# Performance work log

Measured on AMD Instinct MI355X. Metric: run time of the kernel, lower is better.

## Reference

```python
import jax, jax.numpy as jnp
import numpy as np

H = 64  # hidden size

def _lstm_layer(x_btf, w_ih, w_hh, b_ih, b_hh):
    """One LSTM layer, batch_first input x_btf [B,T,F]. PyTorch gate order i,f,g,o."""
    B = x_btf.shape[0]
    # Precompute input contribution for all timesteps: [T,B,4H]
    xg = jnp.einsum('btf,gf->tbg', x_btf, w_ih) + (b_ih + b_hh)
    h0 = jnp.zeros((B, H), dtype=x_btf.dtype)
    c0 = jnp.zeros((B, H), dtype=x_btf.dtype)

    def step(carry, xg_t):
        h, c = carry
        gates = xg_t + h @ w_hh.T  # [B,4H]
        i, f, g, o = jnp.split(gates, 4, axis=-1)
        i = jax.nn.sigmoid(i)
        f = jax.nn.sigmoid(f)
        g = jnp.tanh(g)
        o = jax.nn.sigmoid(o)
        c_new = f * c + i * g
        h_new = o * jnp.tanh(c_new)
        return (h_new, c_new), h_new

    (h_T, c_T), hs = jax.lax.scan(step, (h0, c0), xg)
    return jnp.transpose(hs, (1, 0, 2)), h_T, c_T  # [B,T,H], [B,H], [B,H]


def setup_inputs() -> dict:
    key = jax.random.key(0)
    ks = jax.random.split(key, 9)
    s_in = 1.0 / np.sqrt(H)
    inp = {
        'x': jax.random.normal(ks[0], (512, 2048, 4), dtype=jnp.float32),
        'w_ih_l0': jax.random.uniform(ks[1], (4 * H, 4), jnp.float32, -s_in, s_in),
        'w_hh_l0': jax.random.uniform(ks[2], (4 * H, H), jnp.float32, -s_in, s_in),
        'b_ih_l0': jax.random.uniform(ks[3], (4 * H,), jnp.float32, -s_in, s_in),
        'b_hh_l0': jax.random.uniform(ks[4], (4 * H,), jnp.float32, -s_in, s_in),
        'w_ih_l1': jax.random.uniform(ks[5], (4 * H, H), jnp.float32, -s_in, s_in),
        'w_hh_l1': jax.random.uniform(ks[6], (4 * H, H), jnp.float32, -s_in, s_in),
        'b_ih_l1': jax.random.uniform(ks[7], (4 * H,), jnp.float32, -s_in, s_in),
        'b_hh_l1': jax.random.uniform(ks[8], (4 * H,), jnp.float32, -s_in, s_in),
    }
    return inp


def reference(x, w_ih_l0, w_hh_l0, b_ih_l0, b_hh_l0, w_ih_l1, w_hh_l1, b_ih_l1, b_hh_l1):
    out0, h0, c0 = _lstm_layer(x, w_ih_l0, w_hh_l0, b_ih_l0, b_hh_l0)
    out1, h1, c1 = _lstm_layer(out0, w_ih_l1, w_hh_l1, b_ih_l1, b_hh_l1)
    h_n = jnp.stack([h0, h1], axis=0)  # [num_layers, B, H]
    c_n = jnp.stack([c0, c1], axis=0)
    return out1, (h_n, c_n)
```

## Files before the change

### kernel.cpp

```cpp
#include <hip/hip_runtime.h>

#define T_STEPS 2048
#define HID 64

typedef __attribute__((ext_vector_type(8))) short short8;
typedef __attribute__((ext_vector_type(4))) float f32x4;

static __device__ __forceinline__ unsigned short f2bf(float f) {
    unsigned int uu = __float_as_uint(f);
    uu = uu + 0x7fffu + ((uu >> 16) & 1u);
    return (unsigned short)(uu >> 16);
}
static __device__ __forceinline__ float exp2_f(float x) {
#if __has_builtin(__builtin_amdgcn_exp2f)
    return __builtin_amdgcn_exp2f(x);
#else
    return exp2f(x);
#endif
}
static __device__ __forceinline__ float sig2(float s) {
    return __builtin_amdgcn_rcpf(1.0f + exp2_f(s));
}
static __device__ __forceinline__ float tanh2(float s) {
    return fmaf(2.0f, __builtin_amdgcn_rcpf(1.0f + exp2_f(s)), -1.0f);
}
#define NLOG2E 1.4426950408889634f

__global__ void __launch_bounds__(512, 1) __attribute__((amdgpu_waves_per_eu(2, 2)))
lstm2_ws2(const float* __restrict__ x,
          const float* __restrict__ wih0, const float* __restrict__ whh0,
          const float* __restrict__ bih0, const float* __restrict__ bhh0,
          const float* __restrict__ wih1, const float* __restrict__ whh1,
          const float* __restrict__ bih1, const float* __restrict__ bhh1,
          float* __restrict__ out, int B)
{
    __shared__ __align__(16) unsigned short s_h0[2][2][HID];
    __shared__ __align__(16) unsigned short s_h1[2][2][HID];
    __shared__ __align__(16) float s_xf[2 * T_STEPS * 4];

    const int tid  = threadIdx.x;
    const int lane = tid & 63;
    const int wv   = tid >> 6;
    const int wg   = wv >> 2;
    const int wl   = wv & 3;
    const int l15  = lane & 15;
    const int lg   = lane >> 4;
    const int b0   = 2 * blockIdx.x;
    const int u    = 16 * wl + l15;
    const int bx   = lg & 1;
    const int rsel = (l15 >> 2) & 1;

    const float SCL[4] = {-NLOG2E, -NLOG2E, -2.0f * NLOG2E, -NLOG2E};

    const float4* __restrict__ xb4 = (const float4*)(x + (size_t)b0 * (T_STEPS * 4));
    float4* s_xf4 = (float4*)s_xf;
    for (int i2 = tid; i2 < 2 * T_STEPS; i2 += 512) s_xf4[i2] = xb4[i2];
    if (tid < 256) {
        ((unsigned short*)s_h0)[tid] = 0;
        ((unsigned short*)s_h1)[tid] = 0;
    }

    const size_t BTH = (size_t)B * T_STEPS * HID;
    const size_t BH  = (size_t)B * HID;
    const size_t bi  = (size_t)(b0 + bx) * HID + u;
    const f32x4 Z = {0.f, 0.f, 0.f, 0.f};

    #define BAR() do { asm volatile("s_waitcnt lgkmcnt(0)" ::: "memory"); \
                       __builtin_amdgcn_s_barrier(); } while (0)

    if (wg == 0) {
        short8 W0[4][2];
        float  wx[4][4];
        f32x4  Bias0[4];
        #pragma unroll
        for (int ni = 0; ni < 4; ++ni) {
            const int g = 64 * ni + u;
            const float sc = SCL[ni];
            #pragma unroll
            for (int kt = 0; kt < 2; ++kt)
                #pragma unroll
                for (int j = 0; j < 8; ++j)
                    W0[ni][kt][j] = (short)f2bf(whh0[g * HID + kt * 32 + lg * 8 + j] * sc);
            #pragma unroll
            for (int j = 0; j < 4; ++j) wx[ni][j] = wih0[g * 4 + j] * sc;
            const float bb = (bih0[g] + bhh0[g]) * sc;
            Bias0[ni] = (f32x4){bb, bb, bb, bb};
        }
        float c0s = 0.f, h0s = 0.f;
        const float* xcur = &s_xf[(size_t)bx * T_STEPS * 4];
        __syncthreads();

        auto l0_body = [&](int P) {
            const int Q = P ^ 1;
            const short8 Ha = *(const short8*)&s_h0[Q][rsel][8 * lg];
            const short8 Hb = *(const short8*)&s_h0[Q][rsel][32 + 8 * lg];
            const float4 xt = *(const float4*)xcur;  xcur += 4;
            __builtin_amdgcn_s_setprio(1);
            f32x4 aA0 = __builtin_amdgcn_mfma_f32_16x16x32_bf16(Ha, W0[0][0], Bias0[0], 0, 0, 0);
            f32x4 aA1 = __builtin_amdgcn_mfma_f32_16x16x32_bf16(Ha, W0[1][0], Bias0[1], 0, 0, 0);
            f32x4 aA2 = __builtin_amdgcn_mfma_f32_16x16x32_bf16(Ha, W0[2][0], Bias0[2], 0, 0, 0);
            f32x4 aA3 = __builtin_amdgcn_mfma_f32_16x16x32_bf16(Ha, W0[3][0], Bias0[3], 0, 0, 0);
            f32x4 aB0 = __builtin_amdgcn_mfma_f32_16x16x32_bf16(Hb, W0[0][1], Z, 0, 0, 0);
            f32x4 aB1 = __builtin_amdgcn_mfma_f32_16x16x32_bf16(Hb, W0[1][1], Z, 0, 0, 0);
            f32x4 aB2 = __builtin_amdgcn_mfma_f32_16x16x32_bf16(Hb, W0[2][1], Z, 0, 0, 0);
            f32x4 aB3 = __builtin_amdgcn_mfma_f32_16x16x32_bf16(Hb, W0[3][1], Z, 0, 0, 0);
            __builtin_amdgcn_s_setprio(0);
            float s0 = aA0[0] + aB0[0];
            float s1 = aA1[0] + aB1[0];
            float s2 = aA2[0] + aB2[0];
            float s3 = aA3[0] + aB3[0];
            s0 = fmaf(wx[0][0], xt.x, s0); s0 = fmaf(wx[0][1], xt.y, s0);
            s0 = fmaf(wx[0][2], xt.z, s0); s0 = fmaf(wx[0][3], xt.w, s0);
            s1 = fmaf(wx[1][0], xt.x, s1); s1 = fmaf(wx[1][1], xt.y, s1);
            s1 = fmaf(wx[1][2], xt.z, s1); s1 = fmaf(wx[1][3], xt.w, s1);
            s2 = fmaf(wx[2][0], xt.x, s2); s2 = fmaf(wx[2][1], xt.y, s2);
            s2 = fmaf(wx[2][2], xt.z, s2); s2 = fmaf(wx[2][3], xt.w, s2);
            s3 = fmaf(wx[3][0], xt.x, s3); s3 = fmaf(wx[3][1], xt.y, s3);
            s3 = fmaf(wx[3][2], xt.z, s3); s3 = fmaf(wx[3][3], xt.w, s3);
            float i_ = sig2(s0);
            float f_ = sig2(s1);
            float g_ = tanh2(s2);
            float o_ = sig2(s3);
            c0s = fmaf(f_, c0s, i_ * g_);
            h0s = o_ * tanh2(c0s * (-2.0f * NLOG2E));
            if (lg < 2) s_h0[P][lg][u] = f2bf(h0s);
        };

        for (int it = 0; it < T_STEPS / 2; ++it) {
            l0_body(0); BAR();
            l0_body(1); BAR();
        }
        if (lg < 2) {
            out[BTH + bi]          = h0s;
            out[BTH + 2 * BH + bi] = c0s;
        }
    } else {
        short8 W1[4][4];
        f32x4  Bias1[4];
        #pragma unroll
        for (int ni = 0; ni < 4; ++ni) {
            const int g = 64 * ni + u;
            const float sc = SCL[ni];
            #pragma unroll
            for (int kt = 0; kt < 2; ++kt)
                #pragma unroll
                for (int j = 0; j < 8; ++j) {
                    W1[ni][kt][j]     = (short)f2bf(wih1[g * HID + kt * 32 + lg * 8 + j] * sc);
                    W1[ni][2 + kt][j] = (short)f2bf(whh1[g * HID + kt * 32 + lg * 8 + j] * sc);
                }
            const float bb = (bih1[g] + bhh1[g]) * sc;
            Bias1[ni] = (f32x4){bb, bb, bb, bb};
        }
        float c1s = 0.f, h1s = 0.f;
        float* __restrict__ opp = out + (size_t)(b0 + bx) * T_STEPS * HID + u;
        __syncthreads();
        BAR();

        auto l1_body = [&](int P) {
            const int Q = P ^ 1;
            const short8 Ha = *(const short8*)&s_h0[Q][rsel][8 * lg];
            const short8 Hb = *(const short8*)&s_h0[Q][rsel][32 + 8 * lg];
            const short8 Ga = *(const short8*)&s_h1[Q][rsel][8 * lg];
            const short8 Gb = *(const short8*)&s_h1[Q][rsel][32 + 8 * lg];
            __builtin_amdgcn_s_setprio(1);
            f32x4 dH0 = __builtin_amdgcn_mfma_f32_16x16x32_bf16(Ha, W1[0][0], Bias1[0], 0, 0, 0);
            f32x4 dH1 = __builtin_amdgcn_mfma_f32_16x16x32_bf16(Ha, W1[1][0], Bias1[1], 0, 0, 0);
            f32x4 dH2 = __builtin_amdgcn_mfma_f32_16x16x32_bf16(Ha, W1[2][0], Bias1[2], 0, 0, 0);
            f32x4 dH3 = __builtin_amdgcn_mfma_f32_16x16x32_bf16(Ha, W1[3][0], Bias1[3], 0, 0, 0);
            f32x4 dG0 = __builtin_amdgcn_mfma_f32_16x16x32_bf16(Ga, W1[0][2], Z, 0, 0, 0);
            f32x4 dG1 = __builtin_amdgcn_mfma_f32_16x16x32_bf16(Ga, W1[1][2], Z, 0, 0, 0);
            f32x4 dG2 = __builtin_amdgcn_mfma_f32_16x16x32_bf16(Ga, W1[2][2], Z, 0, 0, 0);
            f32x4 dG3 = __builtin_amdgcn_mfma_f32_16x16x32_bf16(Ga, W1[3][2], Z, 0, 0, 0);
            dH0 = __builtin_amdgcn_mfma_f32_16x16x32_bf16(Hb, W1[0][1], dH0, 0, 0, 0);
            dH1 = __builtin_amdgcn_mfma_f32_16x16x32_bf16(Hb, W1[1][1], dH1, 0, 0, 0);
            dH2 = __builtin_amdgcn_mfma_f32_16x16x32_bf16(Hb, W1[2][1], dH2, 0, 0, 0);
            dH3 = __builtin_amdgcn_mfma_f32_16x16x32_bf16(Hb, W1[3][1], dH3, 0, 0, 0);
            dG0 = __builtin_amdgcn_mfma_f32_16x16x32_bf16(Gb, W1[0][3], dG0, 0, 0, 0);
            dG1 = __builtin_amdgcn_mfma_f32_16x16x32_bf16(Gb, W1[1][3], dG1, 0, 0, 0);
            dG2 = __builtin_amdgcn_mfma_f32_16x16x32_bf16(Gb, W1[2][3], dG2, 0, 0, 0);
            dG3 = __builtin_amdgcn_mfma_f32_16x16x32_bf16(Gb, W1[3][3], dG3, 0, 0, 0);
            __builtin_amdgcn_s_setprio(0);
            float i_ = sig2(dH0[0] + dG0[0]);
            float f_ = sig2(dH1[0] + dG1[0]);
            float g_ = tanh2(dH2[0] + dG2[0]);
            float o_ = sig2(dH3[0] + dG3[0]);
            c1s = fmaf(f_, c1s, i_ * g_);
            h1s = o_ * tanh2(c1s * (-2.0f * NLOG2E));
            if (lg < 2) {
                s_h1[P][lg][u] = f2bf(h1s);
                *opp = h1s;
            }
            opp += HID;
        };

        for (int it = 0; it < T_STEPS / 2 - 1; ++it) {
            l1_body(1); BAR();
            l1_body(0); BAR();
        }
        l1_body(1); BAR();
        l1_body(0);
        if (lg < 2) {
            out[BTH + BH + bi]     = h1s;
            out[BTH + 3 * BH + bi] = c1s;
        }
    }
    #undef BAR
}

extern "C" void kernel_launch(void* const* d_in, const int* in_sizes, int n_in,
                              void* d_out, int out_size, void* d_ws, size_t ws_size,
                              hipStream_t stream) {
    const float* x    = (const float*)d_in[0];
    const float* wih0 = (const float*)d_in[1];
    const float* whh0 = (const float*)d_in[2];
    const float* bih0 = (const float*)d_in[3];
    const float* bhh0 = (const float*)d_in[4];
    const float* wih1 = (const float*)d_in[5];
    const float* whh1 = (const float*)d_in[6];
    const float* bih1 = (const float*)d_in[7];
    const float* bhh1 = (const float*)d_in[8];
    float* out = (float*)d_out;

    const int B = in_sizes[0] / (T_STEPS * 4);

    lstm2_ws2<<<dim3(B / 2), dim3(512), 0, stream>>>(
        x, wih0, whh0, bih0, bhh0, wih1, whh1, bih1, bhh1, out, B);
}
```

Measured before the change: 719.8 us.

## Replace lockstep barriers with LDS counter dataflow sync between LSTM layers

```diff
diff --git a/kernel.cpp b/kernel.cpp
--- a/kernel.cpp
+++ b/kernel.cpp
@@ -27,15 +27,16 @@
 #define NLOG2E 1.4426950408889634f
 
 __global__ void __launch_bounds__(512, 1) __attribute__((amdgpu_waves_per_eu(2, 2)))
-lstm2_ws2(const float* __restrict__ x,
-          const float* __restrict__ wih0, const float* __restrict__ whh0,
-          const float* __restrict__ bih0, const float* __restrict__ bhh0,
-          const float* __restrict__ wih1, const float* __restrict__ whh1,
-          const float* __restrict__ bih1, const float* __restrict__ bhh1,
-          float* __restrict__ out, int B)
+lstm2_df(const float* __restrict__ x,
+         const float* __restrict__ wih0, const float* __restrict__ whh0,
+         const float* __restrict__ bih0, const float* __restrict__ bhh0,
+         const float* __restrict__ wih1, const float* __restrict__ whh1,
+         const float* __restrict__ bih1, const float* __restrict__ bhh1,
+         float* __restrict__ out, int B)
 {
-    __shared__ __align__(16) unsigned short s_h0[2][2][HID];
-    __shared__ __align__(16) unsigned short s_h1[2][2][HID];
+    __shared__ __align__(16) unsigned short s_h0[4][2][HID];
+    __shared__ __align__(16) unsigned short s_h1[4][2][HID];
+    __shared__ __align__(8)  unsigned s_cnt[2];
     __shared__ __align__(16) float s_xf[2 * T_STEPS * 4];
 
     const int tid  = threadIdx.x;
@@ -56,17 +57,34 @@
     float4* s_xf4 = (float4*)s_xf;
     for (int i2 = tid; i2 < 2 * T_STEPS; i2 += 512) s_xf4[i2] = xb4[i2];
     if (tid < 256) {
-        ((unsigned short*)s_h0)[tid] = 0;
-        ((unsigned short*)s_h1)[tid] = 0;
+        ((unsigned short*)s_h0)[tid] = 0; ((unsigned short*)s_h0)[tid + 256] = 0;
+        ((unsigned short*)s_h1)[tid] = 0; ((unsigned short*)s_h1)[tid + 256] = 0;
     }
+    if (tid == 0) { s_cnt[0] = 0; s_cnt[1] = 0; }
+    __syncthreads();
 
     const size_t BTH = (size_t)B * T_STEPS * HID;
     const size_t BH  = (size_t)B * HID;
     const size_t bi  = (size_t)(b0 + bx) * HID + u;
     const f32x4 Z = {0.f, 0.f, 0.f, 0.f};
 
-    #define BAR() do { asm volatile("s_waitcnt lgkmcnt(0)" ::: "memory"); \
-                       __builtin_amdgcn_s_barrier(); } while (0)
+    auto poll2 = [&](int T0, int T1) {
+        if (T0 <= 0 && T1 <= 0) return;
+        const unsigned uT0 = (T0 > 0) ? (unsigned)T0 : 0u;
+        const unsigned uT1 = (T1 > 0) ? (unsigned)T1 : 0u;
+        volatile unsigned long long* pc = (volatile unsigned long long*)&s_cnt[0];
+        unsigned long long cc = *pc;
+        while ((unsigned)cc < uT0 || (unsigned)(cc >> 32) < uT1) {
+            __builtin_amdgcn_s_sleep(1);
+            cc = *pc;
+        }
+        asm volatile("s_waitcnt lgkmcnt(0)" ::: "memory");
+        __builtin_amdgcn_sched_barrier(0);
+    };
+    auto publish = [&](int which) {
+        asm volatile("s_waitcnt lgkmcnt(0)" ::: "memory");
+        if (lane == 0) atomicAdd(&s_cnt[which], 1u);
+    };
 
     if (wg == 0) {
         short8 W0[4][2];
@@ -88,10 +106,10 @@
         }
         float c0s = 0.f, h0s = 0.f;
         const float* xcur = &s_xf[(size_t)bx * T_STEPS * 4];
-        __syncthreads();
-
-        auto l0_body = [&](int P) {
-            const int Q = P ^ 1;
+
+        auto l0_step = [&](int t, int P) {
+            const int Q = (P + 3) & 3;
+            poll2(4 * t, 4 * (t - 3));
             const short8 Ha = *(const short8*)&s_h0[Q][rsel][8 * lg];
             const short8 Hb = *(const short8*)&s_h0[Q][rsel][32 + 8 * lg];
             const float4 xt = *(const float4*)xcur;  xcur += 4;
@@ -124,11 +142,15 @@
             c0s = fmaf(f_, c0s, i_ * g_);
             h0s = o_ * tanh2(c0s * (-2.0f * NLOG2E));
             if (lg < 2) s_h0[P][lg][u] = f2bf(h0s);
+            publish(0);
         };
 
-        for (int it = 0; it < T_STEPS / 2; ++it) {
-            l0_body(0); BAR();
-            l0_body(1); BAR();
+        for (int it = 0; it < T_STEPS / 4; ++it) {
+            const int tb = 4 * it;
+            l0_step(tb + 0, 0);
+            l0_step(tb + 1, 1);
+            l0_step(tb + 2, 2);
+            l0_step(tb + 3, 3);
         }
         if (lg < 2) {
             out[BTH + bi]          = h0s;
@@ -153,13 +175,12 @@
         }
         float c1s = 0.f, h1s = 0.f;
         float* __restrict__ opp = out + (size_t)(b0 + bx) * T_STEPS * HID + u;
-        __syncthreads();
-        BAR();
-
-        auto l1_body = [&](int P) {
-            const int Q = P ^ 1;
-            const short8 Ha = *(const short8*)&s_h0[Q][rsel][8 * lg];
-            const short8 Hb = *(const short8*)&s_h0[Q][rsel][32 + 8 * lg];
+
+        auto l1_step = [&](int s, int P) {
+            const int Q = (P + 3) & 3;
+            poll2(4 * (s + 1), 4 * s);
+            const short8 Ha = *(const short8*)&s_h0[P][rsel][8 * lg];
+            const short8 Hb = *(const short8*)&s_h0[P][rsel][32 + 8 * lg];
             const short8 Ga = *(const short8*)&s_h1[Q][rsel][8 * lg];
             const short8 Gb = *(const short8*)&s_h1[Q][rsel][32 + 8 * lg];
             __builtin_amdgcn_s_setprio(1);
@@ -191,20 +212,21 @@
                 *opp = h1s;
             }
             opp += HID;
+            publish(1);
         };
 
-        for (int it = 0; it < T_STEPS / 2 - 1; ++it) {
-            l1_body(1); BAR();
-            l1_body(0); BAR();
-        }
-        l1_body(1); BAR();
-        l1_body(0);
+        for (int it = 0; it < T_STEPS / 4; ++it) {
+            const int sb = 4 * it;
+            l1_step(sb + 0, 0);
+            l1_step(sb + 1, 1);
+            l1_step(sb + 2, 2);
+            l1_step(sb + 3, 3);
+        }
         if (lg < 2) {
             out[BTH + BH + bi]     = h1s;
             out[BTH + 3 * BH + bi] = c1s;
         }
     }
-    #undef BAR
 }
 
 extern "C" void kernel_launch(void* const* d_in, const int* in_sizes, int n_in,
@@ -223,6 +245,6 @@
 
     const int B = in_sizes[0] / (T_STEPS * 4);
 
-    lstm2_ws2<<<dim3(B / 2), dim3(512), 0, stream>>>(
+    lstm2_df<<<dim3(B / 2), dim3(512), 0, stream>>>(
         x, wih0, whh0, bih0, bhh0, wih1, whh1, bih1, bhh1, out, B);
 }
```

Result: slower. 993.4 us (+38.0%).

## Quantize LSTM recurrent matmuls to int8 MFMA with per-row weight scales

Applied to the files above, without the earlier changes.

```diff
diff --git a/kernel.cpp b/kernel.cpp
--- a/kernel.cpp
+++ b/kernel.cpp
@@ -3,14 +3,9 @@
 #define T_STEPS 2048
 #define HID 64
 
-typedef __attribute__((ext_vector_type(8))) short short8;
+typedef __attribute__((ext_vector_type(4))) int   int4v;
 typedef __attribute__((ext_vector_type(4))) float f32x4;
 
-static __device__ __forceinline__ unsigned short f2bf(float f) {
-    unsigned int uu = __float_as_uint(f);
-    uu = uu + 0x7fffu + ((uu >> 16) & 1u);
-    return (unsigned short)(uu >> 16);
-}
 static __device__ __forceinline__ float exp2_f(float x) {
 #if __has_builtin(__builtin_amdgcn_exp2f)
     return __builtin_amdgcn_exp2f(x);
@@ -18,24 +13,18 @@
     return exp2f(x);
 #endif
 }
-static __device__ __forceinline__ float sig2(float s) {
-    return __builtin_amdgcn_rcpf(1.0f + exp2_f(s));
-}
-static __device__ __forceinline__ float tanh2(float s) {
-    return fmaf(2.0f, __builtin_amdgcn_rcpf(1.0f + exp2_f(s)), -1.0f);
-}
 #define NLOG2E 1.4426950408889634f
 
 __global__ void __launch_bounds__(512, 1) __attribute__((amdgpu_waves_per_eu(2, 2)))
-lstm2_ws2(const float* __restrict__ x,
-          const float* __restrict__ wih0, const float* __restrict__ whh0,
-          const float* __restrict__ bih0, const float* __restrict__ bhh0,
-          const float* __restrict__ wih1, const float* __restrict__ whh1,
-          const float* __restrict__ bih1, const float* __restrict__ bhh1,
-          float* __restrict__ out, int B)
+lstm2_i8(const float* __restrict__ x,
+         const float* __restrict__ wih0, const float* __restrict__ whh0,
+         const float* __restrict__ bih0, const float* __restrict__ bhh0,
+         const float* __restrict__ wih1, const float* __restrict__ whh1,
+         const float* __restrict__ bih1, const float* __restrict__ bhh1,
+         float* __restrict__ out, int B)
 {
-    __shared__ __align__(16) unsigned short s_h0[2][2][HID];
-    __shared__ __align__(16) unsigned short s_h1[2][2][HID];
+    __shared__ __align__(16) char s_h0q[2][2][HID];
+    __shared__ __align__(16) char s_h1q[2][2][HID];
     __shared__ __align__(16) float s_xf[2 * T_STEPS * 4];
 
     const int tid  = threadIdx.x;
@@ -56,35 +45,58 @@
     float4* s_xf4 = (float4*)s_xf;
     for (int i2 = tid; i2 < 2 * T_STEPS; i2 += 512) s_xf4[i2] = xb4[i2];
     if (tid < 256) {
-        ((unsigned short*)s_h0)[tid] = 0;
-        ((unsigned short*)s_h1)[tid] = 0;
+        ((char*)s_h0q)[tid] = 0;
+        ((char*)s_h1q)[tid] = 0;
     }
 
     const size_t BTH = (size_t)B * T_STEPS * HID;
     const size_t BH  = (size_t)B * HID;
     const size_t bi  = (size_t)(b0 + bx) * HID + u;
-    const f32x4 Z = {0.f, 0.f, 0.f, 0.f};
+    const int4v Zi = {0, 0, 0, 0};
+
+    auto pack16 = [&](const float* wr, float qs) {
+        int4v r;
+        #pragma unroll
+        for (int dw = 0; dw < 4; ++dw) {
+            unsigned d = 0;
+            #pragma unroll
+            for (int bbb = 0; bbb < 4; ++bbb) {
+                int q = (int)rintf(wr[dw * 4 + bbb] * qs);
+                d |= ((unsigned)(q & 255)) << (8 * bbb);
+            }
+            r[dw] = (int)d;
+        }
+        return r;
+    };
+    auto rowmax = [&](const float* wr) {
+        float mx = 0.f;
+        #pragma unroll
+        for (int j = 0; j < 16; ++j) mx = fmaxf(mx, fabsf(wr[j]));
+        mx = fmaxf(mx, __shfl_xor(mx, 16));
+        mx = fmaxf(mx, __shfl_xor(mx, 32));
+        return fmaxf(mx, 1e-20f);
+    };
 
     #define BAR() do { asm volatile("s_waitcnt lgkmcnt(0)" ::: "memory"); \
                        __builtin_amdgcn_s_barrier(); } while (0)
 
     if (wg == 0) {
-        short8 W0[4][2];
-        float  wx[4][4];
-        f32x4  Bias0[4];
+        int4v W0q[4];
+        float dq0[4];
+        float wx[4][4];
+        float b0s[4];
         #pragma unroll
         for (int ni = 0; ni < 4; ++ni) {
             const int g = 64 * ni + u;
-            const float sc = SCL[ni];
-            #pragma unroll
-            for (int kt = 0; kt < 2; ++kt)
-                #pragma unroll
-                for (int j = 0; j < 8; ++j)
-                    W0[ni][kt][j] = (short)f2bf(whh0[g * HID + kt * 32 + lg * 8 + j] * sc);
-            #pragma unroll
-            for (int j = 0; j < 4; ++j) wx[ni][j] = wih0[g * 4 + j] * sc;
-            const float bb = (bih0[g] + bhh0[g]) * sc;
-            Bias0[ni] = (f32x4){bb, bb, bb, bb};
+            float wr[16];
+            #pragma unroll
+            for (int j = 0; j < 16; ++j) wr[j] = whh0[g * HID + 16 * lg + j];
+            float mx = rowmax(wr);
+            W0q[ni] = pack16(wr, 127.f / mx);
+            dq0[ni] = (mx / (127.f * 127.f)) * SCL[ni];
+            #pragma unroll
+            for (int j = 0; j < 4; ++j) wx[ni][j] = wih0[g * 4 + j] * SCL[ni];
+            b0s[ni] = (bih0[g] + bhh0[g]) * SCL[ni];
         }
         float c0s = 0.f, h0s = 0.f;
         const float* xcur = &s_xf[(size_t)bx * T_STEPS * 4];
@@ -92,38 +104,33 @@
 
         auto l0_body = [&](int P) {
             const int Q = P ^ 1;
-            const short8 Ha = *(const short8*)&s_h0[Q][rsel][8 * lg];
-            const short8 Hb = *(const short8*)&s_h0[Q][rsel][32 + 8 * lg];
+            const int4v Ha = *(const int4v*)&s_h0q[Q][rsel][16 * lg];
             const float4 xt = *(const float4*)xcur;  xcur += 4;
             __builtin_amdgcn_s_setprio(1);
-            f32x4 aA0 = __builtin_amdgcn_mfma_f32_16x16x32_bf16(Ha, W0[0][0], Bias0[0], 0, 0, 0);
-            f32x4 aA1 = __builtin_amdgcn_mfma_f32_16x16x32_bf16(Ha, W0[1][0], Bias0[1], 0, 0, 0);
-            f32x4 aA2 = __builtin_amdgcn_mfma_f32_16x16x32_bf16(Ha, W0[2][0], Bias0[2], 0, 0, 0);
-            f32x4 aA3 = __builtin_amdgcn_mfma_f32_16x16x32_bf16(Ha, W0[3][0], Bias0[3], 0, 0, 0);
-            f32x4 aB0 = __builtin_amdgcn_mfma_f32_16x16x32_bf16(Hb, W0[0][1], Z, 0, 0, 0);
-            f32x4 aB1 = __builtin_amdgcn_mfma_f32_16x16x32_bf16(Hb, W0[1][1], Z, 0, 0, 0);
-            f32x4 aB2 = __builtin_amdgcn_mfma_f32_16x16x32_bf16(Hb, W0[2][1], Z, 0, 0, 0);
-            f32x4 aB3 = __builtin_amdgcn_mfma_f32_16x16x32_bf16(Hb, W0[3][1], Z, 0, 0, 0);
+            int4v a0 = __builtin_amdgcn_mfma_i32_16x16x64_i8(Ha, W0q[0], Zi, 0, 0, 0);
+            int4v a1 = __builtin_amdgcn_mfma_i32_16x16x64_i8(Ha, W0q[1], Zi, 0, 0, 0);
+            int4v a2 = __builtin_amdgcn_mfma_i32_16x16x64_i8(Ha, W0q[2], Zi, 0, 0, 0);
+            int4v a3 = __builtin_amdgcn_mfma_i32_16x16x64_i8(Ha, W0q[3], Zi, 0, 0, 0);
             __builtin_amdgcn_s_setprio(0);
-            float s0 = aA0[0] + aB0[0];
-            float s1 = aA1[0] + aB1[0];
-            float s2 = aA2[0] + aB2[0];
-            float s3 = aA3[0] + aB3[0];
-            s0 = fmaf(wx[0][0], xt.x, s0); s0 = fmaf(wx[0][1], xt.y, s0);
-            s0 = fmaf(wx[0][2], xt.z, s0); s0 = fmaf(wx[0][3], xt.w, s0);
-            s1 = fmaf(wx[1][0], xt.x, s1); s1 = fmaf(wx[1][1], xt.y, s1);
-            s1 = fmaf(wx[1][2], xt.z, s1); s1 = fmaf(wx[1][3], xt.w, s1);
-            s2 = fmaf(wx[2][0], xt.x, s2); s2 = fmaf(wx[2][1], xt.y, s2);
-            s2 = fmaf(wx[2][2], xt.z, s2); s2 = fmaf(wx[2][3], xt.w, s2);
-            s3 = fmaf(wx[3][0], xt.x, s3); s3 = fmaf(wx[3][1], xt.y, s3);
-            s3 = fmaf(wx[3][2], xt.z, s3); s3 = fmaf(wx[3][3], xt.w, s3);
-            float i_ = sig2(s0);
-            float f_ = sig2(s1);
-            float g_ = tanh2(s2);
-            float o_ = sig2(s3);
+            float t0 = fmaf(wx[0][0], xt.x, b0s[0]);
+            float t1 = fmaf(wx[1][0], xt.x, b0s[1]);
+            float t2 = fmaf(wx[2][0], xt.x, b0s[2]);
+            float t3 = fmaf(wx[3][0], xt.x, b0s[3]);
+            t0 = fmaf(wx[0][1], xt.y, t0); t0 = fmaf(wx[0][2], xt.z, t0); t0 = fmaf(wx[0][3], xt.w, t0);
+            t1 = fmaf(wx[1][1], xt.y, t1); t1 = fmaf(wx[1][2], xt.z, t1); t1 = fmaf(wx[1][3], xt.w, t1);
+            t2 = fmaf(wx[2][1], xt.y, t2); t2 = fmaf(wx[2][2], xt.z, t2); t2 = fmaf(wx[2][3], xt.w, t2);
+            t3 = fmaf(wx[3][1], xt.y, t3); t3 = fmaf(wx[3][2], xt.z, t3); t3 = fmaf(wx[3][3], xt.w, t3);
+            float s0 = fmaf((float)a0[0], dq0[0], t0);
+            float s1 = fmaf((float)a1[0], dq0[1], t1);
+            float s2 = fmaf((float)a2[0], dq0[2], t2);
+            float s3 = fmaf((float)a3[0], dq0[3], t3);
+            float i_ = __builtin_amdgcn_rcpf(1.0f + exp2_f(s0));
+            float f_ = __builtin_amdgcn_rcpf(1.0f + exp2_f(s1));
+            float g_ = fmaf(2.0f, __builtin_amdgcn_rcpf(1.0f + exp2_f(s2)), -1.0f);
+            float o_ = __builtin_amdgcn_rcpf(1.0f + exp2_f(s3));
             c0s = fmaf(f_, c0s, i_ * g_);
-            h0s = o_ * tanh2(c0s * (-2.0f * NLOG2E));
-            if (lg < 2) s_h0[P][lg][u] = f2bf(h0s);
+            h0s = o_ * fmaf(2.0f, __builtin_amdgcn_rcpf(1.0f + exp2_f(c0s * (-2.0f * NLOG2E))), -1.0f);
+            if (lg < 2) s_h0q[P][lg][u] = (char)(int)rintf(h0s * 127.f);
         };
 
         for (int it = 0; it < T_STEPS / 2; ++it) {
@@ -135,21 +142,23 @@
             out[BTH + 2 * BH + bi] = c0s;
         }
     } else {
-        short8 W1[4][4];
-        f32x4  Bias1[4];
+        int4v Wihq[4], Whhq[4];
+        float dqih[4], dqhh[4], b1s[4];
         #pragma unroll
         for (int ni = 0; ni < 4; ++ni) {
             const int g = 64 * ni + u;
-            const float sc = SCL[ni];
-            #pragma unroll
-            for (int kt = 0; kt < 2; ++kt)
-                #pragma unroll
-                for (int j = 0; j < 8; ++j) {
-                    W1[ni][kt][j]     = (short)f2bf(wih1[g * HID + kt * 32 + lg * 8 + j] * sc);
-                    W1[ni][2 + kt][j] = (short)f2bf(whh1[g * HID + kt * 32 + lg * 8 + j] * sc);
-                }
-            const float bb = (bih1[g] + bhh1[g]) * sc;
-            Bias1[ni] = (f32x4){bb, bb, bb, bb};
+            float wr[16];
+            #pragma unroll
+            for (int j = 0; j < 16; ++j) wr[j] = wih1[g * HID + 16 * lg + j];
+            float mxi = rowmax(wr);
+            Wihq[ni] = pack16(wr, 127.f / mxi);
+            dqih[ni] = (mxi / (127.f * 127.f)) * SCL[ni];
+            #pragma unroll
+            for (int j = 0; j < 16; ++j) wr[j] = whh1[g * HID + 16 * lg + j];
+            float mxh = rowmax(wr);
+            Whhq[ni] = pack16(wr, 127.f / mxh);
+            dqhh[ni] = (mxh / (127.f * 127.f)) * SCL[ni];
+            b1s[ni] = (bih1[g] + bhh1[g]) * SCL[ni];
         }
         float c1s = 0.f, h1s = 0.f;
         float* __restrict__ opp = out + (size_t)(b0 + bx) * T_STEPS * HID + u;
@@ -158,36 +167,30 @@
 
         auto l1_body = [&](int P) {
             const int Q = P ^ 1;
-            const short8 Ha = *(const short8*)&s_h0[Q][rsel][8 * lg];
-            const short8 Hb = *(const short8*)&s_h0[Q][rsel][32 + 8 * lg];
-            const short8 Ga = *(const short8*)&s_h1[Q][rsel][8 * lg];
-            const short8 Gb = *(const short8*)&s_h1[Q][rsel][32 + 8 * lg];
+            const int4v Ha = *(const int4v*)&s_h0q[Q][rsel][16 * lg];
+            const int4v Ga = *(const int4v*)&s_h1q[Q][rsel][16 * lg];
             __builtin_amdgcn_s_setprio(1);
-            f32x4 dH0 = __builtin_amdgcn_mfma_f32_16x16x32_bf16(Ha, W1[0][0], Bias1[0], 0, 0, 0);
-            f32x4 dH1 = __builtin_amdgcn_mfma_f32_16x16x32_bf16(Ha, W1[1][0], Bias1[1], 0, 0, 0);
-            f32x4 dH2 = __builtin_amdgcn_mfma_f32_16x16x32_bf16(Ha, W1[2][0], Bias1[2], 0, 0, 0);
-            f32x4 dH3 = __builtin_amdgcn_mfma_f32_16x16x32_bf16(Ha, W1[3][0], Bias1[3], 0, 0, 0);
-            f32x4 dG0 = __builtin_amdgcn_mfma_f32_16x16x32_bf16(Ga, W1[0][2], Z, 0, 0, 0);
-            f32x4 dG1 = __builtin_amdgcn_mfma_f32_16x16x32_bf16(Ga, W1[1][2], Z, 0, 0, 0);
-            f32x4 dG2 = __builtin_amdgcn_mfma_f32_16x16x32_bf16(Ga, W1[2][2], Z, 0, 0, 0);
-            f32x4 dG3 = __builtin_amdgcn_mfma_f32_16x16x32_bf16(Ga, W1[3][2], Z, 0, 0, 0);
-            dH0 = __builtin_amdgcn_mfma_f32_16x16x32_bf16(Hb, W1[0][1], dH0, 0, 0, 0);
-            dH1 = __builtin_amdgcn_mfma_f32_16x16x32_bf16(Hb, W1[1][1], dH1, 0, 0, 0);
-            dH2 = __builtin_amdgcn_mfma_f32_16x16x32_bf16(Hb, W1[2][1], dH2, 0, 0, 0);
-            dH3 = __builtin_amdgcn_mfma_f32_16x16x32_bf16(Hb, W1[3][1], dH3, 0, 0, 0);
-            dG0 = __builtin_amdgcn_mfma_f32_16x16x32_bf16(Gb, W1[0][3], dG0, 0, 0, 0);
-            dG1 = __builtin_amdgcn_mfma_f32_16x16x32_bf16(Gb, W1[1][3], dG1, 0, 0, 0);
-            dG2 = __builtin_amdgcn_mfma_f32_16x16x32_bf16(Gb, W1[2][3], dG2, 0, 0, 0);
-            dG3 = __builtin_amdgcn_mfma_f32_16x16x32_bf16(Gb, W1[3][3], dG3, 0, 0, 0);
+            int4v dH0 = __builtin_amdgcn_mfma_i32_16x16x64_i8(Ha, Wihq[0], Zi, 0, 0, 0);
+            int4v dH1 = __builtin_amdgcn_mfma_i32_16x16x64_i8(Ha, Wihq[1], Zi, 0, 0, 0);
+            int4v dH2 = __builtin_amdgcn_mfma_i32_16x16x64_i8(Ha, Wihq[2], Zi, 0, 0, 0);
+            int4v dH3 = __builtin_amdgcn_mfma_i32_16x16x64_i8(Ha, Wihq[3], Zi, 0, 0, 0);
+            int4v dG0 = __builtin_amdgcn_mfma_i32_16x16x64_i8(Ga, Whhq[0], Zi, 0, 0, 0);
+            int4v dG1 = __builtin_amdgcn_mfma_i32_16x16x64_i8(Ga, Whhq[1], Zi, 0, 0, 0);
+            int4v dG2 = __builtin_amdgcn_mfma_i32_16x16x64_i8(Ga, Whhq[2], Zi, 0, 0, 0);
+            int4v dG3 = __builtin_amdgcn_mfma_i32_16x16x64_i8(Ga, Whhq[3], Zi, 0, 0, 0);
             __builtin_amdgcn_s_setprio(0);
-            float i_ = sig2(dH0[0] + dG0[0]);
-            float f_ = sig2(dH1[0] + dG1[0]);
-            float g_ = tanh2(dH2[0] + dG2[0]);
-            float o_ = sig2(dH3[0] + dG3[0]);
+            float s0 = fmaf((float)dG0[0], dqhh[0], fmaf((float)dH0[0], dqih[0], b1s[0]));
+            float s1 = fmaf((float)dG1[0], dqhh[1], fmaf((float)dH1[0], dqih[1], b1s[1]));
+            float s2 = fmaf((float)dG2[0], dqhh[2], fmaf((float)dH2[0], dqih[2], b1s[2]));
+            float s3 = fmaf((float)dG3[0], dqhh[3], fmaf((float)dH3[0], dqih[3], b1s[3]));
+            float i_ = __builtin_amdgcn_rcpf(1.0f + exp2_f(s0));
+            float f_ = __builtin_amdgcn_rcpf(1.0f + exp2_f(s1));
+            float g_ = fmaf(2.0f, __builtin_amdgcn_rcpf(1.0f + exp2_f(s2)), -1.0f);
+            float o_ = __builtin_amdgcn_rcpf(1.0f + exp2_f(s3));
             c1s = fmaf(f_, c1s, i_ * g_);
-            h1s = o_ * tanh2(c1s * (-2.0f * NLOG2E));
+            h1s = o_ * fmaf(2.0f, __builtin_amdgcn_rcpf(1.0f + exp2_f(c1s * (-2.0f * NLOG2E))), -1.0f);
             if (lg < 2) {
-                s_h1[P][lg][u] = f2bf(h1s);
+                s_h1q[P][lg][u] = (char)(int)rintf(h1s * 127.f);
                 *opp = h1s;
             }
             opp += HID;
@@ -223,6 +226,6 @@
 
     const int B = in_sizes[0] / (T_STEPS * 4);
 
-    lstm2_ws2<<<dim3(B / 2), dim3(512), 0, stream>>>(
+    lstm2_i8<<<dim3(B / 2), dim3(512), 0, stream>>>(
         x, wih0, whh0, bih0, bhh0, wih1, whh1, bih1, bhh1, out, B);
 }
```

New measurement: 649.5 us. -9.8%, faster.
